# Kernel tuning notes

Measured on AMD Instinct MI355X. Metric: run time of the kernel, lower is better.

## Reference

```python
import jax, jax.numpy as jnp
import numpy as np

H = 1024          # hidden_size
NH = 16           # num_attention_heads
HD = H // NH      # head_size
EPS = 1e-5


def setup_inputs() -> dict:
    key = jax.random.key(0)
    ks = jax.random.split(key, 5)
    # xavier_uniform bound for Linear(in, out): sqrt(6/(in+out))
    b_qkv = float(np.sqrt(6.0 / (H + 3 * H)))
    b_out = float(np.sqrt(6.0 / (H + H)))
    return {
        "hidden_states": jax.random.normal(ks[0], (2, 2048, H), dtype=jnp.float32),
        "ln_gamma": jnp.ones((H,), jnp.float32),
        "ln_beta": jnp.zeros((H,), jnp.float32),
        "W_qkv": jax.random.uniform(ks[1], (3 * H, H), jnp.float32, -b_qkv, b_qkv),
        "b_qkv": jnp.zeros((3 * H,), jnp.float32),
        "W_out": jax.random.uniform(ks[2], (H, H), jnp.float32, -b_out, b_out),
        "b_out": jnp.zeros((H,), jnp.float32),
    }


def _attn_block(x, ln_gamma, ln_beta, W_qkv, b_qkv, W_out, b_out):
    B, S, _ = x.shape
    # Pre-LN
    mu = jnp.mean(x, axis=-1, keepdims=True)
    var = jnp.mean(jnp.square(x - mu), axis=-1, keepdims=True)
    xn = (x - mu) / jnp.sqrt(var + EPS) * ln_gamma + ln_beta
    # fused QKV projection: [B,S,3H]
    qkv = jnp.einsum("bsh,oh->bso", xn, W_qkv) + b_qkv
    qkv = qkv.reshape(B, S, 3, NH, HD).transpose(2, 0, 3, 1, 4)  # [3,B,NH,S,HD]
    q, k, v = qkv[0], qkv[1], qkv[2]
    scores = jnp.einsum("bhqd,bhkd->bhqk", q, k) / jnp.sqrt(jnp.asarray(HD, x.dtype))
    probs = jax.nn.softmax(scores, axis=-1)
    ctx = jnp.einsum("bhqk,bhkd->bhqd", probs, v)
    ctx = ctx.transpose(0, 2, 1, 3).reshape(B, S, H)
    out = jnp.einsum("bsh,oh->bso", ctx, W_out) + b_out  # dropout: eval mode = identity
    return x + out


def reference(hidden_states, ln_gamma, ln_beta, W_qkv, b_qkv, W_out, b_out):
    return _attn_block(hidden_states, ln_gamma, ln_beta, W_qkv, b_qkv, W_out, b_out)
```

## Files before the change

### kernel.cpp

```cpp
#include <hip/hip_runtime.h>
#include <stdint.h>

typedef unsigned short u16;
typedef __attribute__((ext_vector_type(8))) short bf16x8;
typedef __attribute__((ext_vector_type(4))) float f32x4;
typedef __attribute__((ext_vector_type(4))) unsigned int u32x4;
typedef __attribute__((ext_vector_type(2))) unsigned int u32x2;
typedef __attribute__((ext_vector_type(4))) unsigned short u16x4;

#define QSCALE 0.18033688011112042f

typedef __attribute__((address_space(1))) const void gvoid;
typedef __attribute__((address_space(3))) void svoid;

__device__ __forceinline__ void cp16(const u16* g, u16* l) {
    __builtin_amdgcn_global_load_lds((gvoid*)g, (svoid*)l, 16, 0, 0);
}

__device__ __forceinline__ u16 f2bf(float f) {
    uint32_t u = __float_as_uint(f);
    u += 0x7fff + ((u >> 16) & 1);
    return (u16)(u >> 16);
}

__device__ __forceinline__ uint32_t pack_bf2(float lo, float hi) {
    uint32_t a = __float_as_uint(lo) + 0x8000u;
    uint32_t b = __float_as_uint(hi) + 0x8000u;
    return __builtin_amdgcn_perm(b, a, 0x07060302);
}

__global__ __launch_bounds__(256) void k_pre(const float* __restrict__ X,
                                             const float* __restrict__ gam,
                                             const float* __restrict__ bet,
                                             u16* __restrict__ XN,
                                             const float* __restrict__ Wqkv, u16* __restrict__ Wq,
                                             const float* __restrict__ Wout, u16* __restrict__ Wo) {
    __shared__ float red[8];
    const int bid = blockIdx.x;
    if (bid < 4096) {
        int t = bid;
        const float4* xp = (const float4*)(X + (size_t)t * 1024);
        float4 x = xp[threadIdx.x];
        float s  = x.x + x.y + x.z + x.w;
        float s2 = x.x*x.x + x.y*x.y + x.z*x.z + x.w*x.w;
        #pragma unroll
        for (int off = 1; off < 64; off <<= 1) {
            s  += __shfl_xor(s,  off, 64);
            s2 += __shfl_xor(s2, off, 64);
        }
        int lane = threadIdx.x & 63, w = threadIdx.x >> 6;
        if (lane == 0) { red[w] = s; red[w + 4] = s2; }
        __syncthreads();
        s  = red[0] + red[1] + red[2] + red[3];
        s2 = red[4] + red[5] + red[6] + red[7];
        float mu  = s * (1.0f / 1024.0f);
        float var = s2 * (1.0f / 1024.0f) - mu * mu;
        float rin = rsqrtf(var + 1e-5f);
        float4 g = ((const float4*)gam)[threadIdx.x];
        float4 b = ((const float4*)bet)[threadIdx.x];
        u16x4 o;
        o.x = f2bf((x.x - mu) * rin * g.x + b.x);
        o.y = f2bf((x.y - mu) * rin * g.y + b.y);
        o.z = f2bf((x.z - mu) * rin * g.z + b.z);
        o.w = f2bf((x.w - mu) * rin * g.w + b.w);
        *(u16x4*)(XN + (size_t)t * 1024 + threadIdx.x * 4) = o;
    } else {
        int i = (bid - 4096) * 256 + threadIdx.x;
        const float* src; u16* dst;
        if (i < 786432) { src = Wqkv; dst = Wq; }
        else            { i -= 786432; src = Wout; dst = Wo; }
        float4 v = ((const float4*)src)[i];
        u16x4 o;
        o.x = f2bf(v.x); o.y = f2bf(v.y); o.z = f2bf(v.z); o.w = f2bf(v.w);
        ((u16x4*)dst)[i] = o;
    }
}

__device__ __forceinline__ void gemm_bt_tile(const u16* __restrict__ A, const u16* __restrict__ Bm,
                                             int m0, int n0, u16* As, u16* Bs, f32x4 acc[4][4]) {
    const int tid = threadIdx.x;
    const int lane = tid & 63;
    const int wv = tid >> 6;
    const int qi = lane & 15, g = lane >> 4, swz = qi & 7;
    const int wr = (wv >> 1) * 64, wc = (wv & 1) * 64;
    #pragma unroll
    for (int mi = 0; mi < 4; mi++)
        #pragma unroll
        for (int ni = 0; ni < 4; ni++) acc[mi][ni] = (f32x4){0.f, 0.f, 0.f, 0.f};

    const int row_in = tid >> 3;
    const int cs = (tid & 7) ^ (row_in & 7);
    for (int k0 = 0; k0 < 1024; k0 += 64) {
        __syncthreads();
        #pragma unroll
        for (int i = 0; i < 4; i++) {
            int row = i * 32 + row_in;
            cp16(A  + (size_t)(m0 + row) * 1024 + k0 + cs * 8, As + (i * 256 + wv * 64) * 8);
            cp16(Bm + (size_t)(n0 + row) * 1024 + k0 + cs * 8, Bs + (i * 256 + wv * 64) * 8);
        }
        __syncthreads();
        #pragma unroll
        for (int ks = 0; ks < 2; ks++) {
            bf16x8 af[4], bf[4];
            #pragma unroll
            for (int mi = 0; mi < 4; mi++)
                af[mi] = *(const bf16x8*)(As + (wr + mi * 16 + qi) * 64 + ((ks * 4 + g) ^ swz) * 8);
            #pragma unroll
            for (int ni = 0; ni < 4; ni++)
                bf[ni] = *(const bf16x8*)(Bs + (wc + ni * 16 + qi) * 64 + ((ks * 4 + g) ^ swz) * 8);
            #pragma unroll
            for (int mi = 0; mi < 4; mi++)
                #pragma unroll
                for (int ni = 0; ni < 4; ni++)
                    acc[mi][ni] = __builtin_amdgcn_mfma_f32_16x16x32_bf16(af[mi], bf[ni], acc[mi][ni], 0, 0, 0);
        }
    }
}

__global__ __launch_bounds__(256) void k_qkv(const u16* __restrict__ XN, const u16* __restrict__ Wq,
                                             const float* __restrict__ bqkv,
                                             u16* __restrict__ Q, u16* __restrict__ K,
                                             u16* __restrict__ Vt) {
    __shared__ __align__(16) u16 SMEM[17408];
    u16* As = SMEM;
    u16* Bs = SMEM + 8192;
    f32x4 acc[4][4];
    const int m0 = blockIdx.y * 128, n0 = blockIdx.x * 128;
    gemm_bt_tile(XN, Wq, m0, n0, As, Bs, acc);
    const int lane = threadIdx.x & 63, wid = threadIdx.x >> 6;
    const int g = lane >> 4, qi = lane & 15;
    const int wr = (wid >> 1) * 64, wc = (wid & 1) * 64;
    if (n0 < 2048) {
        const int which = n0 >> 10;
        u16* base = which ? K : Q;
        const float scale = which ? 1.0f : QSCALE;
        #pragma unroll
        for (int mi = 0; mi < 4; mi++)
            #pragma unroll
            for (int ni = 0; ni < 4; ni++)
                #pragma unroll
                for (int i = 0; i < 4; i++) {
                    int m = m0 + wr + mi * 16 + (g * 4 + i);
                    int n = n0 + wc + ni * 16 + qi;
                    float v = (acc[mi][ni][i] + bqkv[n]) * scale;
                    int b = m >> 11, s = m & 2047;
                    int hh = (n >> 6) & 15, d = n & 63;
                    base[((size_t)(b * 16 + hh) * 2048 + s) * 64 + d] = f2bf(v);
                }
    } else {
        __syncthreads();
        u16* Tw = SMEM + wid * 4352;
        #pragma unroll
        for (int mi = 0; mi < 4; mi++)
            #pragma unroll
            for (int ni = 0; ni < 4; ni++) {
                int n = n0 + wc + ni * 16 + qi;
                float bq = bqkv[n];
                u16x4 pk;
                pk.x = f2bf(acc[mi][ni][0] + bq);
                pk.y = f2bf(acc[mi][ni][1] + bq);
                pk.z = f2bf(acc[mi][ni][2] + bq);
                pk.w = f2bf(acc[mi][ni][3] + bq);
                *(u16x4*)(Tw + (ni * 16 + qi) * 68 + mi * 16 + g * 4) = pk;
            }
        const int head = (n0 + wc - 2048) >> 6;
        const int b = m0 >> 11;
        const int s0 = (m0 + wr) & 2047;
        u16* vrow = Vt + (size_t)(b * 16 + head) * 64 * 2048 + s0 + qi * 4;
        #pragma unroll
        for (int dd = 0; dd < 16; dd++) {
            int d = dd * 4 + g;
            u16x4 val = *(const u16x4*)(Tw + d * 68 + qi * 4);
            *(u16x4*)(vrow + (size_t)d * 2048) = val;
        }
    }
}

__global__ __launch_bounds__(256) void k_attn(const u16* __restrict__ Q, const u16* __restrict__ K,
                                              const u16* __restrict__ Vt, u16* __restrict__ CTX) {
    __shared__ __align__(16) u16 Ks[2][64 * 64];
    __shared__ __align__(16) u16 Vs[2][64 * 64];
    __shared__ __align__(16) u16 Ps[4][32 * 64];
    const int id = blockIdx.x;
    const int bh = (id & 7) * 4 + ((id >> 3) & 3);
    const int q0 = (id >> 5) * 128;
    const int lane = threadIdx.x & 63, w = threadIdx.x >> 6;
    const int g = lane >> 4, qi = lane & 15, swz = qi & 7;
    const u16* Qp = Q  + (size_t)bh * (2048 * 64);
    const u16* Kp = K  + (size_t)bh * (2048 * 64);
    const u16* Vp = Vt + (size_t)bh * (64 * 2048);
    u16* Pw = Ps[w];

    const int r0 = threadIdx.x >> 3;
    const int cs = (threadIdx.x & 7) ^ (r0 & 7);
    const u16* kg0 = Kp + (size_t)r0 * 64 + cs * 8;
    const u16* kg1 = kg0 + 32 * 64;
    const u16* vg0 = Vp + (size_t)r0 * 2048 + cs * 8;
    const u16* vg1 = vg0 + 32 * 2048;

    bf16x8 bq[2][2];
    #pragma unroll
    for (int f = 0; f < 2; f++) {
        const u16* qb = Qp + (size_t)(q0 + w * 32 + f * 16 + qi) * 64 + g * 8;
        bq[f][0] = *(const bf16x8*)(qb);
        bq[f][1] = *(const bf16x8*)(qb + 32);
    }
    float lsum0 = 0.f, lsum1 = 0.f;
    f32x4 od[2][4];
    #pragma unroll
    for (int f = 0; f < 2; f++)
        #pragma unroll
        for (int nt = 0; nt < 4; nt++) od[f][nt] = (f32x4){0.f, 0.f, 0.f, 0.f};

    cp16(kg0, Ks[0] + w * 512);
    cp16(kg1, Ks[0] + 2048 + w * 512);
    cp16(vg0, Vs[0] + w * 512);
    cp16(vg1, Vs[0] + 2048 + w * 512);

    #define ATTN_STEP(KT, CKS, CVS, PKS, PVS)                                                    \
    {                                                                                            \
        const int kt_ = (KT);                                                                    \
        __syncthreads();                                                                         \
        if (kt_ < 31) {                                                                          \
            cp16(kg0 + 4096, (PKS) + w * 512);                                                   \
            cp16(kg1 + 4096, (PKS) + 2048 + w * 512);                                            \
            cp16(vg0 + 64,   (PVS) + w * 512);                                                   \
            cp16(vg1 + 64,   (PVS) + 2048 + w * 512);                                            \
        }                                                                                        \
        const u16* ksp = (CKS);                                                                  \
        const u16* vsp = (CVS);                                                                  \
        f32x4 sv[2][4];                                                                          \
        _Pragma("unroll")                                                                        \
        for (int f = 0; f < 2; f++)                                                              \
            _Pragma("unroll")                                                                    \
            for (int nt = 0; nt < 4; nt++) sv[f][nt] = (f32x4){0.f, 0.f, 0.f, 0.f};              \
        _Pragma("unroll")                                                                        \
        for (int ks = 0; ks < 2; ks++)                                                           \
            _Pragma("unroll")                                                                    \
            for (int nt = 0; nt < 4; nt++) {                                                     \
                bf16x8 ak = *(const bf16x8*)(ksp + (nt * 16 + qi) * 64 + ((ks * 4 + g) ^ swz) * 8); \
                sv[0][nt] = __builtin_amdgcn_mfma_f32_16x16x32_bf16(ak, bq[0][ks], sv[0][nt], 0, 0, 0); \
                sv[1][nt] = __builtin_amdgcn_mfma_f32_16x16x32_bf16(ak, bq[1][ks], sv[1][nt], 0, 0, 0); \
            }                                                                                    \
        _Pragma("unroll")                                                                        \
        for (int f = 0; f < 2; f++)                                                              \
            _Pragma("unroll")                                                                    \
            for (int nt = 0; nt < 2; nt++) {                                                     \
                float e0 = __builtin_amdgcn_exp2f(sv[f][nt][0]);                                 \
                float e1 = __builtin_amdgcn_exp2f(sv[f][nt][1]);                                 \
                float e2 = __builtin_amdgcn_exp2f(sv[f][nt][2]);                                 \
                float e3 = __builtin_amdgcn_exp2f(sv[f][nt][3]);                                 \
                if (f == 0) lsum0 += (e0 + e1) + (e2 + e3); else lsum1 += (e0 + e1) + (e2 + e3); \
                u32x2 pk = {pack_bf2(e0, e1), pack_bf2(e2, e3)};                                 \
                *(u32x2*)(Pw + (f * 16 + qi) * 64 + ((2 * nt + (g >> 1)) ^ swz) * 8 + (g & 1) * 4) = pk; \
            }                                                                                    \
        {                                                                                        \
            bf16x8 bp0 = *(const bf16x8*)(Pw + qi * 64 + (g ^ swz) * 8);                         \
            bf16x8 bp1 = *(const bf16x8*)(Pw + (16 + qi) * 64 + (g ^ swz) * 8);                  \
            _Pragma("unroll")                                                                    \
            for (int nt = 0; nt < 4; nt++) {                                                     \
                bf16x8 av = *(const bf16x8*)(vsp + (nt * 16 + qi) * 64 + (g ^ swz) * 8);         \
                od[0][nt] = __builtin_amdgcn_mfma_f32_16x16x32_bf16(av, bp0, od[0][nt], 0, 0, 0); \
                od[1][nt] = __builtin_amdgcn_mfma_f32_16x16x32_bf16(av, bp1, od[1][nt], 0, 0, 0); \
            }                                                                                    \
        }                                                                                        \
        _Pragma("unroll")                                                                        \
        for (int f = 0; f < 2; f++)                                                              \
            _Pragma("unroll")                                                                    \
            for (int nt = 2; nt < 4; nt++) {                                                     \
                float e0 = __builtin_amdgcn_exp2f(sv[f][nt][0]);                                 \
                float e1 = __builtin_amdgcn_exp2f(sv[f][nt][1]);                                 \
                float e2 = __builtin_amdgcn_exp2f(sv[f][nt][2]);                                 \
                float e3 = __builtin_amdgcn_exp2f(sv[f][nt][3]);                                 \
                if (f == 0) lsum0 += (e0 + e1) + (e2 + e3); else lsum1 += (e0 + e1) + (e2 + e3); \
                u32x2 pk = {pack_bf2(e0, e1), pack_bf2(e2, e3)};                                 \
                *(u32x2*)(Pw + (f * 16 + qi) * 64 + ((2 * nt + (g >> 1)) ^ swz) * 8 + (g & 1) * 4) = pk; \
            }                                                                                    \
        {                                                                                        \
            bf16x8 bp0 = *(const bf16x8*)(Pw + qi * 64 + ((4 + g) ^ swz) * 8);                   \
            bf16x8 bp1 = *(const bf16x8*)(Pw + (16 + qi) * 64 + ((4 + g) ^ swz) * 8);            \
            _Pragma("unroll")                                                                    \
            for (int nt = 0; nt < 4; nt++) {                                                     \
                bf16x8 av = *(const bf16x8*)(vsp + (nt * 16 + qi) * 64 + ((4 + g) ^ swz) * 8);   \
                od[0][nt] = __builtin_amdgcn_mfma_f32_16x16x32_bf16(av, bp0, od[0][nt], 0, 0, 0); \
                od[1][nt] = __builtin_amdgcn_mfma_f32_16x16x32_bf16(av, bp1, od[1][nt], 0, 0, 0); \
            }                                                                                    \
        }                                                                                        \
        kg0 += 4096; kg1 += 4096; vg0 += 64; vg1 += 64;                                          \
    }

    for (int kt = 0; kt < 32; kt += 2) {
        ATTN_STEP(kt,     Ks[0], Vs[0], Ks[1], Vs[1]);
        ATTN_STEP(kt + 1, Ks[1], Vs[1], Ks[0], Vs[0]);
    }
    #undef ATTN_STEP

    lsum0 += __shfl_xor(lsum0, 16, 64);
    lsum0 += __shfl_xor(lsum0, 32, 64);
    lsum1 += __shfl_xor(lsum1, 16, 64);
    lsum1 += __shfl_xor(lsum1, 32, 64);
    const float inv[2] = {1.0f / lsum0, 1.0f / lsum1};
    const int b = bh >> 4, hh = bh & 15;
    #pragma unroll
    for (int f = 0; f < 2; f++) {
        size_t m = (size_t)b * 2048 + q0 + w * 32 + f * 16 + qi;
        u16* cp = CTX + m * 1024 + hh * 64 + g * 4;
        #pragma unroll
        for (int nt = 0; nt < 4; nt++) {
            u16x4 o;
            o.x = f2bf(od[f][nt][0] * inv[f]); o.y = f2bf(od[f][nt][1] * inv[f]);
            o.z = f2bf(od[f][nt][2] * inv[f]); o.w = f2bf(od[f][nt][3] * inv[f]);
            *(u16x4*)(cp + nt * 16) = o;
        }
    }
}

__global__ __launch_bounds__(256) void k_out(const u16* __restrict__ CTX, const u16* __restrict__ Wo,
                                             const float* __restrict__ bout, const float* __restrict__ X,
                                             float* __restrict__ OUT) {
    __shared__ __align__(16) u16 As[128 * 64], Bs[128 * 64];
    f32x4 acc[4][4];
    const int m0 = blockIdx.y * 128, n0 = blockIdx.x * 128;
    gemm_bt_tile(CTX, Wo, m0, n0, As, Bs, acc);
    const int lane = threadIdx.x & 63, wid = threadIdx.x >> 6;
    const int wr = (wid >> 1) * 64, wc = (wid & 1) * 64;
    #pragma unroll
    for (int mi = 0; mi < 4; mi++)
        #pragma unroll
        for (int ni = 0; ni < 4; ni++)
            #pragma unroll
            for (int i = 0; i < 4; i++) {
                size_t m = m0 + wr + mi * 16 + ((lane >> 4) * 4 + i);
                int n = n0 + wc + ni * 16 + (lane & 15);
                OUT[m * 1024 + n] = acc[mi][ni][i] + bout[n] + X[m * 1024 + n];
            }
}

extern "C" void kernel_launch(void* const* d_in, const int* in_sizes, int n_in,
                              void* d_out, int out_size, void* d_ws, size_t ws_size,
                              hipStream_t stream) {
    const float* X    = (const float*)d_in[0];
    const float* gam  = (const float*)d_in[1];
    const float* bet  = (const float*)d_in[2];
    const float* Wqkv = (const float*)d_in[3];
    const float* bqkv = (const float*)d_in[4];
    const float* Wout = (const float*)d_in[5];
    const float* bout = (const float*)d_in[6];
    float* OUT = (float*)d_out;

    u16* XN  = (u16*)d_ws;
    u16* Q   = XN  + (size_t)4 * 1024 * 1024;
    u16* K   = Q   + (size_t)4 * 1024 * 1024;
    u16* Vt  = K   + (size_t)4 * 1024 * 1024;
    u16* CTX = Vt  + (size_t)4 * 1024 * 1024;
    u16* Wq  = CTX + (size_t)4 * 1024 * 1024;
    u16* Wo  = Wq  + (size_t)3 * 1024 * 1024;

    k_pre<<<8192, 256, 0, stream>>>(X, gam, bet, XN, Wqkv, Wq, Wout, Wo);
    k_qkv<<<dim3(24, 32), 256, 0, stream>>>(XN, Wq, bqkv, Q, K, Vt);
    k_attn<<<512, 256, 0, stream>>>(Q, K, Vt, CTX);
    k_out<<<dim3(8, 32), 256, 0, stream>>>(CTX, Wo, bout, X, OUT);
}
```

Measured before the change: 204.1 us.

## Split attention along keys into two halves and merge with a reduction kernel

```diff
diff --git a/kernel.cpp b/kernel.cpp
--- a/kernel.cpp
+++ b/kernel.cpp
@@ -21,6 +21,10 @@
     uint32_t u = __float_as_uint(f);
     u += 0x7fff + ((u >> 16) & 1);
     return (u16)(u >> 16);
+}
+
+__device__ __forceinline__ float bf2f(u16 u) {
+    return __uint_as_float(((uint32_t)u) << 16);
 }
 
 __device__ __forceinline__ uint32_t pack_bf2(float lo, float hi) {
@@ -177,13 +181,16 @@
 }
 
 __global__ __launch_bounds__(256) void k_attn(const u16* __restrict__ Q, const u16* __restrict__ K,
-                                              const u16* __restrict__ Vt, u16* __restrict__ CTX) {
+                                              const u16* __restrict__ Vt,
+                                              u16* __restrict__ OP0, u16* __restrict__ OP1,
+                                              float* __restrict__ LS) {
     __shared__ __align__(16) u16 Ks[2][64 * 64];
     __shared__ __align__(16) u16 Vs[2][64 * 64];
     __shared__ __align__(16) u16 Ps[4][32 * 64];
     const int id = blockIdx.x;
     const int bh = (id & 7) * 4 + ((id >> 3) & 3);
-    const int q0 = (id >> 5) * 128;
+    const int q0 = ((id >> 5) & 15) * 128;
+    const int half = id >> 9;
     const int lane = threadIdx.x & 63, w = threadIdx.x >> 6;
     const int g = lane >> 4, qi = lane & 15, swz = qi & 7;
     const u16* Qp = Q  + (size_t)bh * (2048 * 64);
@@ -193,9 +200,9 @@
 
     const int r0 = threadIdx.x >> 3;
     const int cs = (threadIdx.x & 7) ^ (r0 & 7);
-    const u16* kg0 = Kp + (size_t)r0 * 64 + cs * 8;
+    const u16* kg0 = Kp + (size_t)(half * 1024 + r0) * 64 + cs * 8;
     const u16* kg1 = kg0 + 32 * 64;
-    const u16* vg0 = Vp + (size_t)r0 * 2048 + cs * 8;
+    const u16* vg0 = Vp + (size_t)r0 * 2048 + half * 1024 + cs * 8;
     const u16* vg1 = vg0 + 32 * 2048;
 
     bf16x8 bq[2][2];
@@ -221,7 +228,7 @@
     {                                                                                            \
         const int kt_ = (KT);                                                                    \
         __syncthreads();                                                                         \
-        if (kt_ < 31) {                                                                          \
+        if (kt_ < 15) {                                                                          \
             cp16(kg0 + 4096, (PKS) + w * 512);                                                   \
             cp16(kg1 + 4096, (PKS) + 2048 + w * 512);                                            \
             cp16(vg0 + 64,   (PVS) + w * 512);                                                   \
@@ -289,7 +296,7 @@
         kg0 += 4096; kg1 += 4096; vg0 += 64; vg1 += 64;                                          \
     }
 
-    for (int kt = 0; kt < 32; kt += 2) {
+    for (int kt = 0; kt < 16; kt += 2) {
         ATTN_STEP(kt,     Ks[0], Vs[0], Ks[1], Vs[1]);
         ATTN_STEP(kt + 1, Ks[1], Vs[1], Ks[0], Vs[0]);
     }
@@ -299,20 +306,40 @@
     lsum0 += __shfl_xor(lsum0, 32, 64);
     lsum1 += __shfl_xor(lsum1, 16, 64);
     lsum1 += __shfl_xor(lsum1, 32, 64);
-    const float inv[2] = {1.0f / lsum0, 1.0f / lsum1};
-    const int b = bh >> 4, hh = bh & 15;
+    u16* OPh = half ? OP1 : OP0;
+    const size_t pbase = (size_t)bh * 2048;
     #pragma unroll
     for (int f = 0; f < 2; f++) {
-        size_t m = (size_t)b * 2048 + q0 + w * 32 + f * 16 + qi;
-        u16* cp = CTX + m * 1024 + hh * 64 + g * 4;
+        int q = q0 + w * 32 + f * 16 + qi;
+        u16* op = OPh + (pbase + q) * 64 + g * 4;
         #pragma unroll
         for (int nt = 0; nt < 4; nt++) {
             u16x4 o;
-            o.x = f2bf(od[f][nt][0] * inv[f]); o.y = f2bf(od[f][nt][1] * inv[f]);
-            o.z = f2bf(od[f][nt][2] * inv[f]); o.w = f2bf(od[f][nt][3] * inv[f]);
-            *(u16x4*)(cp + nt * 16) = o;
-        }
-    }
+            o.x = f2bf(od[f][nt][0]); o.y = f2bf(od[f][nt][1]);
+            o.z = f2bf(od[f][nt][2]); o.w = f2bf(od[f][nt][3]);
+            *(u16x4*)(op + nt * 16) = o;
+        }
+        if (g == 0) LS[(size_t)half * 65536 + pbase + q] = (f == 0) ? lsum0 : lsum1;
+    }
+}
+
+__global__ __launch_bounds__(256) void k_red(const u16* __restrict__ OP0, const u16* __restrict__ OP1,
+                                             const float* __restrict__ LS, u16* __restrict__ CTX) {
+    int i4 = blockIdx.x * 256 + threadIdx.x;
+    int e = i4 * 4;
+    int m = e >> 10, col = e & 1023;
+    int hh = col >> 6, d = col & 63;
+    int b = m >> 11, q = m & 2047;
+    size_t r = (size_t)(b * 16 + hh) * 2048 + q;
+    u16x4 a0 = *(const u16x4*)(OP0 + r * 64 + d);
+    u16x4 a1 = *(const u16x4*)(OP1 + r * 64 + d);
+    float inv = 1.0f / (LS[r] + LS[65536 + r]);
+    u16x4 o;
+    o.x = f2bf((bf2f(a0.x) + bf2f(a1.x)) * inv);
+    o.y = f2bf((bf2f(a0.y) + bf2f(a1.y)) * inv);
+    o.z = f2bf((bf2f(a0.z) + bf2f(a1.z)) * inv);
+    o.w = f2bf((bf2f(a0.w) + bf2f(a1.w)) * inv);
+    *(u16x4*)(CTX + (size_t)m * 1024 + col) = o;
 }
 
 __global__ __launch_bounds__(256) void k_out(const u16* __restrict__ CTX, const u16* __restrict__ Wo,
@@ -355,9 +382,13 @@
     u16* CTX = Vt  + (size_t)4 * 1024 * 1024;
     u16* Wq  = CTX + (size_t)4 * 1024 * 1024;
     u16* Wo  = Wq  + (size_t)3 * 1024 * 1024;
+    u16* OP0 = XN;
+    u16* OP1 = Wo  + (size_t)1024 * 1024;
+    float* LS = (float*)Wq;
 
     k_pre<<<8192, 256, 0, stream>>>(X, gam, bet, XN, Wqkv, Wq, Wout, Wo);
     k_qkv<<<dim3(24, 32), 256, 0, stream>>>(XN, Wq, bqkv, Q, K, Vt);
-    k_attn<<<512, 256, 0, stream>>>(Q, K, Vt, CTX);
+    k_attn<<<1024, 256, 0, stream>>>(Q, K, Vt, OP0, OP1, LS);
+    k_red<<<4096, 256, 0, stream>>>(OP0, OP1, LS, CTX);
     k_out<<<dim3(8, 32), 256, 0, stream>>>(CTX, Wo, bout, X, OUT);
 }
```

New measurement: 211.9 us. +3.8%, slower.
